# Kernel optimization log

Hardware: AMD Instinct MI355X
Metric: run time of the kernel (lower is better)

The kernel has to match this reference:

```python
import jax, jax.numpy as jnp
import numpy as np

DIM = 1024
D_STATE = 16
D_CONV = 4
EXPAND = 2
D_INNER = EXPAND * DIM          # 2048
DT_RANK = DIM // 16             # 64 (mamba default: ceil(d_model/16))
BATCH = 2
SEQ = 2048


def setup_inputs() -> dict:
    key = jax.random.key(0)
    ks = jax.random.split(key, 32)
    s = 0.02
    def mk(k, shape):
        return jax.random.normal(k, shape, jnp.float32) * s
    inp = {}
    inp["hidden_state"] = jax.random.normal(ks[0], (BATCH, SEQ, DIM), jnp.float32)
    inp["mask"] = jax.random.bernoulli(ks[1], 0.7, (BATCH, SEQ)).astype(jnp.float32)
    inp["mask_proj_w"] = mk(ks[2], (DIM, 1))
    inp["mask_proj_b"] = mk(ks[3], (DIM,))
    i = 4
    A_init = jnp.log(jnp.broadcast_to(jnp.arange(1, D_STATE + 1, dtype=jnp.float32), (D_INNER, D_STATE)))
    for p in ("f", "b"):
        inp[p + "_in_w"]   = mk(ks[i], (2 * D_INNER, DIM)); i += 1
        inp[p + "_conv_w"] = mk(ks[i], (D_INNER, D_CONV)); i += 1
        inp[p + "_conv_b"] = mk(ks[i], (D_INNER,)); i += 1
        inp[p + "_xproj_w"] = mk(ks[i], (DT_RANK + 2 * D_STATE, D_INNER)); i += 1
        inp[p + "_dt_w"]   = mk(ks[i], (D_INNER, DT_RANK)); i += 1
        inp[p + "_dt_b"]   = mk(ks[i], (D_INNER,)) + 1.0  # softplus(~1) -> moderate dt
        i += 1
        inp[p + "_A_log"]  = A_init
        inp[p + "_D"]      = jnp.ones((D_INNER,), jnp.float32)
        inp[p + "_out_w"]  = mk(ks[i], (DIM, D_INNER)); i += 1
    return inp


def _mamba(x, in_w, conv_w, conv_b, xproj_w, dt_w, dt_b, A_log, Dp, out_w):
    # x: [B, L, DIM]
    Bsz = x.shape[0]
    xz = x @ in_w.T                                  # [B, L, 2*D_INNER]
    xi, z = jnp.split(xz, 2, axis=-1)
    # causal depthwise conv1d over time
    xc = jnp.transpose(xi, (0, 2, 1))                # [B, D_INNER, L]
    xc = jax.lax.conv_general_dilated(
        xc, conv_w[:, None, :], window_strides=(1,),
        padding=[(D_CONV - 1, 0)], feature_group_count=D_INNER)
    xc = xc + conv_b[None, :, None]
    u = jax.nn.silu(jnp.transpose(xc, (0, 2, 1)))    # [B, L, D_INNER]
    dbc = u @ xproj_w.T                              # [B, L, DT_RANK + 2*D_STATE]
    dt, Bm, Cm = jnp.split(dbc, [DT_RANK, DT_RANK + D_STATE], axis=-1)
    delta = jax.nn.softplus(dt @ dt_w.T + dt_b)      # [B, L, D_INNER]
    A = -jnp.exp(A_log)                              # [D_INNER, D_STATE]
    dA = jnp.exp(jnp.einsum('bld,dn->bldn', delta, A))
    dBu = jnp.einsum('bld,bln,bld->bldn', delta, Bm, u)
    def step(h, inps):
        dA_t, dBu_t, C_t = inps                      # [B,D_INNER,D_STATE], [B,D_INNER,D_STATE], [B,D_STATE]
        h = dA_t * h + dBu_t
        y = jnp.einsum('bdn,bn->bd', h, C_t)
        return h, y
    h0 = jnp.zeros((Bsz, D_INNER, D_STATE), x.dtype)
    xs = (jnp.moveaxis(dA, 1, 0), jnp.moveaxis(dBu, 1, 0), jnp.moveaxis(Cm, 1, 0))
    _, ys = jax.lax.scan(step, h0, xs)               # ys: [L, B, D_INNER]
    y = jnp.moveaxis(ys, 0, 1) + u * Dp              # [B, L, D_INNER]
    y = y * jax.nn.silu(z)
    return y @ out_w.T                               # [B, L, DIM]


def reference(hidden_state, mask, mask_proj_w, mask_proj_b,
              f_in_w, f_conv_w, f_conv_b, f_xproj_w, f_dt_w, f_dt_b, f_A_log, f_D, f_out_w,
              b_in_w, b_conv_w, b_conv_b, b_xproj_w, b_dt_w, b_dt_b, b_A_log, b_D, b_out_w):
    m = mask[..., None]                              # [B, L, 1]
    mask_features = m @ mask_proj_w.T + mask_proj_b  # [B, L, DIM]
    x_masked = hidden_state * m + mask_features * (1.0 - m)
    forward_out = _mamba(x_masked, f_in_w, f_conv_w, f_conv_b, f_xproj_w,
                         f_dt_w, f_dt_b, f_A_log, f_D, f_out_w)
    backward_out = jnp.flip(
        _mamba(jnp.flip(x_masked, 1), b_in_w, b_conv_w, b_conv_b, b_xproj_w,
               b_dt_w, b_dt_b, b_A_log, b_D, b_out_w), 1)
    ssm_output = forward_out + backward_out
    return ssm_output * m + hidden_state * (1.0 - m)
```

## Files before the change

### kernel.cpp

```cpp
#include <hip/hip_runtime.h>
#include <hip/hip_bf16.h>
#include <stdint.h>

typedef unsigned short u16;
using bf16x8 = __attribute__((ext_vector_type(8))) short;
using f32x4  = __attribute__((ext_vector_type(4))) float;
typedef unsigned short u16x4 __attribute__((ext_vector_type(4)));

#define AS1 __attribute__((address_space(1)))
#define AS3 __attribute__((address_space(3)))

__device__ __forceinline__ float bf2f(u16 x) {
    union { unsigned int u; float f; } v; v.u = ((unsigned int)x) << 16; return v.f;
}
__device__ __forceinline__ u16 f2bf(float f) {
    union { float f; unsigned int u; } v; v.f = f;
    return (u16)((v.u + 0x7fffu + ((v.u >> 16) & 1u)) >> 16);
}

#define ACT_NONE 0
#define ACT_SOFTPLUS 1

__global__ __launch_bounds__(256) void gemm_bt_kernel(
    const u16* __restrict__ A, int lda,
    const u16* __restrict__ B,
    float* __restrict__ Cf, u16* __restrict__ Cb,
    const float* __restrict__ bias,
    int ldc, int M, int N, int K, int Nreal,
    int act, int kSlices,
    const float* __restrict__ hid, const float* __restrict__ msk)
{
    __shared__ __align__(16) u16 As[128 * 64];
    __shared__ __align__(16) u16 Bs[128 * 64];

    const int tid  = threadIdx.x;
    const int bm   = blockIdx.y * 128;
    const int bn   = blockIdx.x * 128;
    const int lane = tid & 63;
    const int wid  = tid >> 6;
    const int wr   = (wid >> 1) * 64;
    const int wc   = (wid & 1) * 64;
    const int l15  = lane & 15;
    const int l4   = lane >> 4;

    const int kLen = K / kSlices;
    const int kt0  = (blockIdx.z * kLen) >> 6;
    const int nK   = kLen >> 6;

    f32x4 acc[4][4];
    const f32x4 vzero = {0.f, 0.f, 0.f, 0.f};
    #pragma unroll
    for (int i = 0; i < 4; ++i)
        #pragma unroll
        for (int j = 0; j < 4; ++j) acc[i][j] = vzero;

    for (int t = 0; t < nK; ++t) {
        int kt = kt0 + t;
        #pragma unroll
        for (int i = 0; i < 4; ++i) {
            int off  = i * 4096 + tid * 16;
            int row  = off >> 7;
            int colB = off & 127;
            const char* src = (const char*)A + ((size_t)(bm + row) * lda + ((size_t)kt << 6)) * 2 + colB;
            __builtin_amdgcn_global_load_lds((const AS1 unsigned int*)src,
                                             (AS3 unsigned int*)((char*)As + off), 16, 0, 0);
        }
        #pragma unroll
        for (int i = 0; i < 4; ++i) {
            int off  = i * 4096 + tid * 16;
            int row  = off >> 7;
            int colB = off & 127;
            const char* src = (const char*)B + ((size_t)(bn + row) * K + ((size_t)kt << 6)) * 2 + colB;
            __builtin_amdgcn_global_load_lds((const AS1 unsigned int*)src,
                                             (AS3 unsigned int*)((char*)Bs + off), 16, 0, 0);
        }
        __syncthreads();

        #pragma unroll
        for (int kk = 0; kk < 2; ++kk) {
            bf16x8 af[4], bfr[4];
            #pragma unroll
            for (int mt = 0; mt < 4; ++mt) {
                int row = wr + mt * 16 + l15;
                af[mt] = *(const bf16x8*)((const char*)As + row * 128 + kk * 64 + l4 * 16);
            }
            #pragma unroll
            for (int nt = 0; nt < 4; ++nt) {
                int row = wc + nt * 16 + l15;
                bfr[nt] = *(const bf16x8*)((const char*)Bs + row * 128 + kk * 64 + l4 * 16);
            }
            #pragma unroll
            for (int mt = 0; mt < 4; ++mt)
                #pragma unroll
                for (int nt = 0; nt < 4; ++nt)
                    acc[mt][nt] = __builtin_amdgcn_mfma_f32_16x16x32_bf16(
                        af[mt], bfr[nt], acc[mt][nt], 0, 0, 0);
        }
        __syncthreads();
    }

    #pragma unroll
    for (int mt = 0; mt < 4; ++mt) {
        #pragma unroll
        for (int nt = 0; nt < 4; ++nt) {
            int col = bn + wc + nt * 16 + l15;
            if (col >= Nreal) continue;
            #pragma unroll
            for (int r = 0; r < 4; ++r) {
                int rw = bm + wr + mt * 16 + l4 * 4 + r;
                float v = acc[mt][nt][r];
                if (act == ACT_SOFTPLUS) {
                    v += bias[col];
                    v = fmaxf(v, 0.f) + log1pf(__expf(-fabsf(v)));
                }
                size_t ci = (size_t)rw * ldc + col;
                if (kSlices > 1) {
                    atomicAdd(&Cf[ci], v);
                } else if (hid) {
                    float m = msk[rw];
                    Cf[ci] = v * m + hid[ci] * (1.f - m);
                } else if (Cb) {
                    Cb[ci] = f2bf(v);
                } else {
                    Cf[ci] = v;
                }
            }
        }
    }
}

template<int REV>
__global__ void conv_silu_kernel(const u16* __restrict__ x,
                                 const float* __restrict__ cw,
                                 const float* __restrict__ cb,
                                 u16* __restrict__ u)
{
    int d  = blockIdx.x * 256 + threadIdx.x;
    int r0 = blockIdx.y * 16;
    float w0 = cw[d*4+0], w1 = cw[d*4+1], w2 = cw[d*4+2], w3 = cw[d*4+3];
    float bias = cb[d];
    if (!REV) {
        float x1, x2, x3;
        if (r0 & 2047) {
            x1 = bf2f(x[(size_t)(r0-1) * 8192 + d]);
            x2 = bf2f(x[(size_t)(r0-2) * 8192 + d]);
            x3 = bf2f(x[(size_t)(r0-3) * 8192 + d]);
        } else { x1 = x2 = x3 = 0.f; }
        #pragma unroll
        for (int i = 0; i < 16; ++i) {
            int r = r0 + i;
            float x0 = bf2f(x[(size_t)r * 8192 + d]);
            float acc = fmaf(w3, x0, fmaf(w2, x1, fmaf(w1, x2, fmaf(w0, x3, bias))));
            float sig = 1.f / (1.f + __expf(-acc));
            u[(size_t)r * 2048 + d] = f2bf(acc * sig);
            x3 = x2; x2 = x1; x1 = x0;
        }
    } else {
        int le = (r0 + 15) & 2047;
        float x1, x2, x3;
        x1 = (le + 1 < 2048) ? bf2f(x[(size_t)(r0+16) * 8192 + d]) : 0.f;
        x2 = (le + 2 < 2048) ? bf2f(x[(size_t)(r0+17) * 8192 + d]) : 0.f;
        x3 = (le + 3 < 2048) ? bf2f(x[(size_t)(r0+18) * 8192 + d]) : 0.f;
        #pragma unroll
        for (int i = 15; i >= 0; --i) {
            int r = r0 + i;
            float x0 = bf2f(x[(size_t)r * 8192 + d]);
            float acc = fmaf(w3, x0, fmaf(w2, x1, fmaf(w1, x2, fmaf(w0, x3, bias))));
            float sig = 1.f / (1.f + __expf(-acc));
            u[(size_t)r * 2048 + d] = f2bf(acc * sig);
            x3 = x2; x2 = x1; x1 = x0;
        }
    }
}

#define NCH 32
#define CSZ 64
#define SUB 16
#define LW  264

template<int REV>
__global__ __launch_bounds__(256) void scan_part1(
    const u16* __restrict__ delta, const u16* __restrict__ u,
    const float* __restrict__ dbc, const float* __restrict__ A_log,
    float* __restrict__ P, float* __restrict__ S)
{
    __shared__ __align__(16) u16   dl_s[SUB * LW];
    __shared__ __align__(16) u16   ul_s[SUB * LW];
    __shared__ __align__(16) float b_s[SUB * 16];

    const int tid = threadIdx.x;
    const int d0  = blockIdx.x * 256;
    const int c   = blockIdx.y;
    const int b   = blockIdx.z;
    const int d   = d0 + tid;
    const size_t rbase = (size_t)b * 2048 + c * CSZ;

    float a2[16], h[16], p[16];
    #pragma unroll
    for (int q = 0; q < 4; ++q) {
        float4 al = *(const float4*)&A_log[(size_t)d * 16 + q * 4];
        a2[q*4+0] = -__expf(al.x) * 1.4426950408889634f;
        a2[q*4+1] = -__expf(al.y) * 1.4426950408889634f;
        a2[q*4+2] = -__expf(al.z) * 1.4426950408889634f;
        a2[q*4+3] = -__expf(al.w) * 1.4426950408889634f;
    }
    #pragma unroll
    for (int n = 0; n < 16; ++n) { h[n] = 0.f; p[n] = 1.f; }

    const int sr  = tid >> 4;
    const int sc16 = (tid & 15) * 16;

    for (int sch = 0; sch < CSZ / SUB; ++sch) {
        const int sch_ = REV ? (CSZ / SUB - 1 - sch) : sch;
        {
            size_t row = rbase + sch_ * SUB + sr;
            *(bf16x8*)&dl_s[sr * LW + sc16]     = *(const bf16x8*)&delta[row * 2048 + d0 + sc16];
            *(bf16x8*)&dl_s[sr * LW + sc16 + 8] = *(const bf16x8*)&delta[row * 2048 + d0 + sc16 + 8];
            *(bf16x8*)&ul_s[sr * LW + sc16]     = *(const bf16x8*)&u[row * 2048 + d0 + sc16];
            *(bf16x8*)&ul_s[sr * LW + sc16 + 8] = *(const bf16x8*)&u[row * 2048 + d0 + sc16 + 8];
            if (tid < 64) {
                int r2 = tid >> 2, c4 = (tid & 3) * 4;
                size_t g2 = rbase + sch_ * SUB + r2;
                *(float4*)&b_s[r2 * 16 + c4] = *(const float4*)&dbc[g2 * 96 + 64 + c4];
            }
        }
        __syncthreads();
        for (int s = 0; s < SUB; ++s) {
            const int s_ = REV ? (SUB - 1 - s) : s;
            float dv  = bf2f(dl_s[s_ * LW + tid]);
            float uv  = bf2f(ul_s[s_ * LW + tid]);
            float dvu = dv * uv;
            const float4* Bp = (const float4*)&b_s[s_ * 16];
            #pragma unroll
            for (int q = 0; q < 4; ++q) {
                float4 Bq = Bp[q];
                #pragma unroll
                for (int j = 0; j < 4; ++j) {
                    int n = q * 4 + j;
                    float dA = exp2f(dv * a2[n]);
                    h[n] = fmaf(dA, h[n], dvu * ((&Bq.x)[j]));
                    p[n] *= dA;
                }
            }
        }
        __syncthreads();
    }

    size_t base = (((size_t)(b * NCH + c)) << 15) + (size_t)d * 16;
    #pragma unroll
    for (int q = 0; q < 4; ++q) {
        float4 pv = { p[q*4+0], p[q*4+1], p[q*4+2], p[q*4+3] };
        float4 sv = { h[q*4+0], h[q*4+1], h[q*4+2], h[q*4+3] };
        *(float4*)&P[base + q * 4] = pv;
        *(float4*)&S[base + q * 4] = sv;
    }
}

template<int REV>
__global__ void scan_part2(const float* __restrict__ P, float* __restrict__ S)
{
    int i  = blockIdx.x * 256 + threadIdx.x;
    int b  = i >> 15;
    int dn = i & 32767;
    size_t base = ((size_t)b * NCH) << 15;
    float h = 0.f;
    #pragma unroll 4
    for (int cc = 0; cc < NCH; ++cc) {
        int c = REV ? (NCH - 1 - cc) : cc;
        size_t idx = base + ((size_t)c << 15) + dn;
        float p = P[idx];
        float s = S[idx];
        S[idx] = h;
        h = fmaf(p, h, s);
    }
}

template<int REV>
__global__ __launch_bounds__(256) void scan_part3(
    const u16* __restrict__ delta, const u16* __restrict__ u,
    const float* __restrict__ dbc, const u16* __restrict__ z,
    const float* __restrict__ A_log, const float* __restrict__ Dp,
    const float* __restrict__ Hin, u16* __restrict__ y)
{
    __shared__ __align__(16) u16   dl_s[SUB * LW];
    __shared__ __align__(16) u16   ul_s[SUB * LW];
    __shared__ __align__(16) u16   zl_s[SUB * LW];
    __shared__ __align__(16) float bc_s[SUB * 32];

    const int tid = threadIdx.x;
    const int d0  = blockIdx.x * 256;
    const int c   = blockIdx.y;
    const int b   = blockIdx.z;
    const int d   = d0 + tid;
    const size_t rbase = (size_t)b * 2048 + c * CSZ;

    float a2[16], h[16];
    #pragma unroll
    for (int q = 0; q < 4; ++q) {
        float4 al = *(const float4*)&A_log[(size_t)d * 16 + q * 4];
        a2[q*4+0] = -__expf(al.x) * 1.4426950408889634f;
        a2[q*4+1] = -__expf(al.y) * 1.4426950408889634f;
        a2[q*4+2] = -__expf(al.z) * 1.4426950408889634f;
        a2[q*4+3] = -__expf(al.w) * 1.4426950408889634f;
    }
    {
        size_t base = (((size_t)(b * NCH + c)) << 15) + (size_t)d * 16;
        #pragma unroll
        for (int q = 0; q < 4; ++q) {
            float4 hv = *(const float4*)&Hin[base + q * 4];
            h[q*4+0] = hv.x; h[q*4+1] = hv.y; h[q*4+2] = hv.z; h[q*4+3] = hv.w;
        }
    }
    const float Dd = Dp[d];

    const int sr   = tid >> 4;
    const int sc16 = (tid & 15) * 16;

    for (int sch = 0; sch < CSZ / SUB; ++sch) {
        const int sch_ = REV ? (CSZ / SUB - 1 - sch) : sch;
        {
            size_t row = rbase + sch_ * SUB + sr;
            *(bf16x8*)&dl_s[sr * LW + sc16]     = *(const bf16x8*)&delta[row * 2048 + d0 + sc16];
            *(bf16x8*)&dl_s[sr * LW + sc16 + 8] = *(const bf16x8*)&delta[row * 2048 + d0 + sc16 + 8];
            *(bf16x8*)&ul_s[sr * LW + sc16]     = *(const bf16x8*)&u[row * 2048 + d0 + sc16];
            *(bf16x8*)&ul_s[sr * LW + sc16 + 8] = *(const bf16x8*)&u[row * 2048 + d0 + sc16 + 8];
            *(bf16x8*)&zl_s[sr * LW + sc16]     = *(const bf16x8*)&z[row * 8192 + d0 + sc16];
            *(bf16x8*)&zl_s[sr * LW + sc16 + 8] = *(const bf16x8*)&z[row * 8192 + d0 + sc16 + 8];
            if (tid < 128) {
                int r2 = tid >> 3, c4 = (tid & 7) * 4;
                size_t g2 = rbase + sch_ * SUB + r2;
                *(float4*)&bc_s[r2 * 32 + c4] = *(const float4*)&dbc[g2 * 96 + 64 + c4];
            }
        }
        __syncthreads();
        for (int s = 0; s < SUB; ++s) {
            const int s_ = REV ? (SUB - 1 - s) : s;
            float dv  = bf2f(dl_s[s_ * LW + tid]);
            float uv  = bf2f(ul_s[s_ * LW + tid]);
            float dvu = dv * uv;
            float yv  = 0.f;
            const float4* Bp = (const float4*)&bc_s[s_ * 32];
            const float4* Cp = (const float4*)&bc_s[s_ * 32 + 16];
            #pragma unroll
            for (int q = 0; q < 4; ++q) {
                float4 Bq = Bp[q];
                float4 Cq = Cp[q];
                #pragma unroll
                for (int j = 0; j < 4; ++j) {
                    int n = q * 4 + j;
                    float dA = exp2f(dv * a2[n]);
                    h[n] = fmaf(dA, h[n], dvu * ((&Bq.x)[j]));
                    yv   = fmaf(h[n], ((&Cq.x)[j]), yv);
                }
            }
            float zv  = bf2f(zl_s[s_ * LW + tid]);
            float sig = 1.f / (1.f + __expf(-zv));
            float out = (yv + uv * Dd) * (zv * sig);
            y[(rbase + sch_ * SUB + s_) * 4096 + d] = f2bf(out);
        }
        __syncthreads();
    }
}

__global__ void blend_kernel(const float* __restrict__ hidden, const float* __restrict__ mask,
                             const float* __restrict__ mw, const float* __restrict__ mb,
                             u16* __restrict__ xm)
{
    size_t i = (size_t)blockIdx.x * 256 + threadIdx.x;
    int r = (int)(i >> 10), c = (int)(i & 1023);
    float m = mask[r];
    float v = hidden[i] * m + (m * mw[c] + mb[c]) * (1.f - m);
    xm[i] = f2bf(v);
}

struct CvtArgs { const float* src[8]; u16* dst[8]; };
__global__ void cvt_weights_kernel(CvtArgs a)
{
    size_t i = (size_t)blockIdx.x * 256 + threadIdx.x;
    if (i < 8388608) {
        int s = (int)(i >> 22);
        size_t j = i & 4194303;
        a.dst[0][i] = f2bf(a.src[s][j]);
    } else if (i < 12582912) {
        size_t k = i - 8388608;
        int s = (int)(k >> 21);
        size_t j = k & 2097151;
        int n = (int)(j >> 11), kk = (int)(j & 2047);
        a.dst[2][(size_t)n * 4096 + s * 2048 + kk] = f2bf(a.src[2 + s][j]);
    } else if (i < 12845056) {
        size_t k = i - 12582912;
        int s = 4 + (int)(k >> 17);
        size_t j = k & 131071;
        a.dst[s][j] = f2bf(a.src[s][j]);
    } else if (i < 13369344) {
        size_t k = i - 12845056;
        int s = 6 + (int)(k >> 18);
        size_t j = k & 262143;
        int r = (int)(j >> 11), c = (int)(j & 2047);
        a.dst[s][j] = (r < 96) ? f2bf(a.src[s][(size_t)r * 2048 + c]) : (u16)0;
    }
}

__global__ void cvt_dt_kernel(const float* __restrict__ dbc, u16* __restrict__ dst) {
    int i = blockIdx.x * 256 + threadIdx.x;
    int r = i >> 6, c = i & 63;
    dst[i] = f2bf(dbc[(size_t)r * 96 + c]);
}

extern "C" void kernel_launch(void* const* d_in, const int* in_sizes, int n_in,
                              void* d_out, int out_size, void* d_ws, size_t ws_size,
                              hipStream_t stream)
{
    (void)in_sizes; (void)n_in; (void)out_size; (void)ws_size;
    const float* hidden = (const float*)d_in[0];
    const float* mask   = (const float*)d_in[1];
    const float* mpw    = (const float*)d_in[2];
    const float* mpb    = (const float*)d_in[3];

    char* ws = (char*)d_ws;
    size_t off = 0;
    auto alloc = [&](size_t bytes) -> char* {
        char* p = ws + off; off += (bytes + 255) & ~(size_t)255; return p;
    };
    u16*   xm     = (u16*)  alloc(4096ull * 1024 * 2);
    u16*   xz     = (u16*)  alloc(4096ull * 8192 * 2);
    u16*   ub     = (u16*)  alloc(4096ull * 2048 * 2);
    float* dbc    = (float*)alloc(4096ull * 96 * 4);
    u16*   dtb    = (u16*)  alloc(4096ull * 64 * 2);
    u16*   delta  = (u16*)  alloc(4096ull * 2048 * 2);
    u16*   yb     = (u16*)  alloc(4096ull * 4096 * 2);
    float* Pbuf   = (float*)alloc(2ull * NCH * 2048 * 16 * 4);
    float* Sbuf   = (float*)alloc(2ull * NCH * 2048 * 16 * 4);
    u16*   w_in   = (u16*)  alloc(8192ull * 1024 * 2);
    u16*   w_out  = (u16*)  alloc(1024ull * 4096 * 2);
    u16*   w_xp[2] = { (u16*)alloc(128ull*2048*2), (u16*)alloc(128ull*2048*2) };
    u16*   w_dt[2] = { (u16*)alloc(2048ull*64*2),  (u16*)alloc(2048ull*64*2)  };

    {
        CvtArgs ca;
        ca.src[0] = (const float*)d_in[4];  ca.src[1] = (const float*)d_in[13];
        ca.src[2] = (const float*)d_in[12]; ca.src[3] = (const float*)d_in[21];
        ca.src[4] = (const float*)d_in[8];  ca.src[5] = (const float*)d_in[17];
        ca.src[6] = (const float*)d_in[7];  ca.src[7] = (const float*)d_in[16];
        ca.dst[0] = w_in;  ca.dst[1] = nullptr;
        ca.dst[2] = w_out; ca.dst[3] = nullptr;
        ca.dst[4] = w_dt[0]; ca.dst[5] = w_dt[1];
        ca.dst[6] = w_xp[0]; ca.dst[7] = w_xp[1];
        cvt_weights_kernel<<<(13369344 + 255) / 256, 256, 0, stream>>>(ca);
    }
    blend_kernel<<<16384, 256, 0, stream>>>(hidden, mask, mpw, mpb, xm);

    gemm_bt_kernel<<<dim3(64, 32, 1), 256, 0, stream>>>(
        xm, 1024, w_in, nullptr, xz, nullptr, 8192, 4096, 8192, 1024, 8192,
        ACT_NONE, 1, nullptr, nullptr);

    for (int dir = 0; dir < 2; ++dir) {
        int base = 4 + dir * 9;
        const float* conv_w = (const float*)d_in[base+1];
        const float* conv_b = (const float*)d_in[base+2];
        const float* dt_b   = (const float*)d_in[base+5];
        const float* A_log  = (const float*)d_in[base+6];
        const float* Dp     = (const float*)d_in[base+7];
        const u16* xi = xz + dir * 4096;
        const u16* zp = xz + dir * 4096 + 2048;

        if (dir == 0) conv_silu_kernel<0><<<dim3(8, 256), 256, 0, stream>>>(xi, conv_w, conv_b, ub);
        else          conv_silu_kernel<1><<<dim3(8, 256), 256, 0, stream>>>(xi, conv_w, conv_b, ub);

        hipMemsetAsync(dbc, 0, 4096ull * 96 * 4, stream);
        gemm_bt_kernel<<<dim3(1, 32, 4), 256, 0, stream>>>(
            ub, 2048, w_xp[dir], dbc, nullptr, nullptr, 96, 4096, 128, 2048, 96,
            ACT_NONE, 4, nullptr, nullptr);
        cvt_dt_kernel<<<(4096*64)/256, 256, 0, stream>>>(dbc, dtb);
        gemm_bt_kernel<<<dim3(16, 32, 1), 256, 0, stream>>>(
            dtb, 64, w_dt[dir], nullptr, delta, dt_b, 2048, 4096, 2048, 64, 2048,
            ACT_SOFTPLUS, 1, nullptr, nullptr);

        u16* yd = yb + dir * 2048;
        if (dir == 0) {
            scan_part1<0><<<dim3(8, NCH, 2), 256, 0, stream>>>(delta, ub, dbc, A_log, Pbuf, Sbuf);
            scan_part2<0><<<256, 256, 0, stream>>>(Pbuf, Sbuf);
            scan_part3<0><<<dim3(8, NCH, 2), 256, 0, stream>>>(delta, ub, dbc, zp, A_log, Dp, Sbuf, yd);
        } else {
            scan_part1<1><<<dim3(8, NCH, 2), 256, 0, stream>>>(delta, ub, dbc, A_log, Pbuf, Sbuf);
            scan_part2<1><<<256, 256, 0, stream>>>(Pbuf, Sbuf);
            scan_part3<1><<<dim3(8, NCH, 2), 256, 0, stream>>>(delta, ub, dbc, zp, A_log, Dp, Sbuf, yd);
        }
    }

    gemm_bt_kernel<<<dim3(8, 32, 1), 256, 0, stream>>>(
        yb, 4096, w_out, (float*)d_out, nullptr, nullptr, 1024, 4096, 1024, 4096, 1024,
        ACT_NONE, 1, hidden, mask);
}
```

Baseline: 763.1 us.

## Batch forward and backward directions into single dual-direction kernel launches

Merges the per-direction conv, x-proj GEMM, dt GEMM and three scan kernels into launches that cover both directions through the grid z dimension. It also folds the blend into the weight-conversion kernel and writes delta into the unused xi slot of xz. The aim is to cut launch count and raise occupancy for the small under-filled kernels such as the scan, x-proj and part2. The cost is duplicated buffers for u, dbc and P/S, plus per-block pointer selection logic.

```diff
diff --git a/kernel.cpp b/kernel.cpp
--- a/kernel.cpp
+++ b/kernel.cpp
@@ -5,7 +5,6 @@
 typedef unsigned short u16;
 using bf16x8 = __attribute__((ext_vector_type(8))) short;
 using f32x4  = __attribute__((ext_vector_type(4))) float;
-typedef unsigned short u16x4 __attribute__((ext_vector_type(4)));
 
 #define AS1 __attribute__((address_space(1)))
 #define AS3 __attribute__((address_space(3)))
@@ -20,6 +19,11 @@
 
 #define ACT_NONE 0
 #define ACT_SOFTPLUS 1
+
+struct GemmSel {
+    const u16* A1; const u16* B1;
+    float* Cf1; u16* Cb1; const float* bias1;
+};
 
 __global__ __launch_bounds__(256) void gemm_bt_kernel(
     const u16* __restrict__ A, int lda,
@@ -27,8 +31,9 @@
     float* __restrict__ Cf, u16* __restrict__ Cb,
     const float* __restrict__ bias,
     int ldc, int M, int N, int K, int Nreal,
-    int act, int kSlices,
-    const float* __restrict__ hid, const float* __restrict__ msk)
+    int act, int kSlices, int zDiv,
+    const float* __restrict__ hid, const float* __restrict__ msk,
+    GemmSel sel)
 {
     __shared__ __align__(16) u16 As[128 * 64];
     __shared__ __align__(16) u16 Bs[128 * 64];
@@ -43,8 +48,16 @@
     const int l15  = lane & 15;
     const int l4   = lane >> 4;
 
+    const int dir   = blockIdx.z / zDiv;
+    const int slice = blockIdx.z % zDiv;
+    const u16* Ap = (dir && sel.A1) ? sel.A1 : A;
+    const u16* Bp = (dir && sel.B1) ? sel.B1 : B;
+    float* CfP = (dir && sel.Cf1) ? sel.Cf1 : Cf;
+    u16*   CbP = (dir && sel.Cb1) ? sel.Cb1 : Cb;
+    const float* biasP = (dir && sel.bias1) ? sel.bias1 : bias;
+
     const int kLen = K / kSlices;
-    const int kt0  = (blockIdx.z * kLen) >> 6;
+    const int kt0  = (slice * kLen) >> 6;
     const int nK   = kLen >> 6;
 
     f32x4 acc[4][4];
@@ -61,7 +74,7 @@
             int off  = i * 4096 + tid * 16;
             int row  = off >> 7;
             int colB = off & 127;
-            const char* src = (const char*)A + ((size_t)(bm + row) * lda + ((size_t)kt << 6)) * 2 + colB;
+            const char* src = (const char*)Ap + ((size_t)(bm + row) * lda + ((size_t)kt << 6)) * 2 + colB;
             __builtin_amdgcn_global_load_lds((const AS1 unsigned int*)src,
                                              (AS3 unsigned int*)((char*)As + off), 16, 0, 0);
         }
@@ -70,7 +83,7 @@
             int off  = i * 4096 + tid * 16;
             int row  = off >> 7;
             int colB = off & 127;
-            const char* src = (const char*)B + ((size_t)(bn + row) * K + ((size_t)kt << 6)) * 2 + colB;
+            const char* src = (const char*)Bp + ((size_t)(bn + row) * K + ((size_t)kt << 6)) * 2 + colB;
             __builtin_amdgcn_global_load_lds((const AS1 unsigned int*)src,
                                              (AS3 unsigned int*)((char*)Bs + off), 16, 0, 0);
         }
@@ -110,36 +123,39 @@
                 int rw = bm + wr + mt * 16 + l4 * 4 + r;
                 float v = acc[mt][nt][r];
                 if (act == ACT_SOFTPLUS) {
-                    v += bias[col];
+                    v += biasP[col];
                     v = fmaxf(v, 0.f) + log1pf(__expf(-fabsf(v)));
                 }
                 size_t ci = (size_t)rw * ldc + col;
                 if (kSlices > 1) {
-                    atomicAdd(&Cf[ci], v);
+                    atomicAdd(&CfP[ci], v);
                 } else if (hid) {
                     float m = msk[rw];
-                    Cf[ci] = v * m + hid[ci] * (1.f - m);
-                } else if (Cb) {
-                    Cb[ci] = f2bf(v);
+                    CfP[ci] = v * m + hid[ci] * (1.f - m);
+                } else if (CbP) {
+                    CbP[ci] = f2bf(v);
                 } else {
-                    Cf[ci] = v;
+                    CfP[ci] = v;
                 }
             }
         }
     }
 }
 
-template<int REV>
-__global__ void conv_silu_kernel(const u16* __restrict__ x,
-                                 const float* __restrict__ cw,
-                                 const float* __restrict__ cb,
-                                 u16* __restrict__ u)
-{
+struct ConvArgs { const float* cw[2]; const float* cb[2]; u16* u[2]; };
+__global__ void conv_silu_dual(const u16* __restrict__ xz, ConvArgs a)
+{
+    const int dir = blockIdx.z;
+    const u16* x = xz + dir * 4096;
+    const float* cw = a.cw[dir];
+    const float* cb = a.cb[dir];
+    u16* u = a.u[dir];
+
     int d  = blockIdx.x * 256 + threadIdx.x;
     int r0 = blockIdx.y * 16;
     float w0 = cw[d*4+0], w1 = cw[d*4+1], w2 = cw[d*4+2], w3 = cw[d*4+3];
     float bias = cb[d];
-    if (!REV) {
+    if (dir == 0) {
         float x1, x2, x3;
         if (r0 & 2047) {
             x1 = bf2f(x[(size_t)(r0-1) * 8192 + d]);
@@ -178,11 +194,18 @@
 #define SUB 16
 #define LW  264
 
-template<int REV>
-__global__ __launch_bounds__(256) void scan_part1(
-    const u16* __restrict__ delta, const u16* __restrict__ u,
-    const float* __restrict__ dbc, const float* __restrict__ A_log,
-    float* __restrict__ P, float* __restrict__ S)
+struct ScanArgs {
+    const u16* delta[2];
+    const u16* u[2];
+    const float* dbc[2];
+    const u16* z[2];
+    const float* Alog[2];
+    const float* Dp[2];
+    float* P[2]; float* S[2];
+    u16* y[2];
+};
+
+__global__ __launch_bounds__(256) void scan_part1_dual(ScanArgs sa)
 {
     __shared__ __align__(16) u16   dl_s[SUB * LW];
     __shared__ __align__(16) u16   ul_s[SUB * LW];
@@ -191,14 +214,20 @@
     const int tid = threadIdx.x;
     const int d0  = blockIdx.x * 256;
     const int c   = blockIdx.y;
-    const int b   = blockIdx.z;
+    const int dir = blockIdx.z >> 1;
+    const int b   = blockIdx.z & 1;
+    const int rev = dir;
     const int d   = d0 + tid;
     const size_t rbase = (size_t)b * 2048 + c * CSZ;
+
+    const u16* D = sa.delta[dir];
+    const u16* U = sa.u[dir];
+    const float* BC = sa.dbc[dir];
 
     float a2[16], h[16], p[16];
     #pragma unroll
     for (int q = 0; q < 4; ++q) {
-        float4 al = *(const float4*)&A_log[(size_t)d * 16 + q * 4];
+        float4 al = *(const float4*)&sa.Alog[dir][(size_t)d * 16 + q * 4];
         a2[q*4+0] = -__expf(al.x) * 1.4426950408889634f;
         a2[q*4+1] = -__expf(al.y) * 1.4426950408889634f;
         a2[q*4+2] = -__expf(al.z) * 1.4426950408889634f;
@@ -211,22 +240,22 @@
     const int sc16 = (tid & 15) * 16;
 
     for (int sch = 0; sch < CSZ / SUB; ++sch) {
-        const int sch_ = REV ? (CSZ / SUB - 1 - sch) : sch;
+        const int sch_ = rev ? (CSZ / SUB - 1 - sch) : sch;
         {
             size_t row = rbase + sch_ * SUB + sr;
-            *(bf16x8*)&dl_s[sr * LW + sc16]     = *(const bf16x8*)&delta[row * 2048 + d0 + sc16];
-            *(bf16x8*)&dl_s[sr * LW + sc16 + 8] = *(const bf16x8*)&delta[row * 2048 + d0 + sc16 + 8];
-            *(bf16x8*)&ul_s[sr * LW + sc16]     = *(const bf16x8*)&u[row * 2048 + d0 + sc16];
-            *(bf16x8*)&ul_s[sr * LW + sc16 + 8] = *(const bf16x8*)&u[row * 2048 + d0 + sc16 + 8];
+            *(bf16x8*)&dl_s[sr * LW + sc16]     = *(const bf16x8*)&D[row * 8192 + d0 + sc16];
+            *(bf16x8*)&dl_s[sr * LW + sc16 + 8] = *(const bf16x8*)&D[row * 8192 + d0 + sc16 + 8];
+            *(bf16x8*)&ul_s[sr * LW + sc16]     = *(const bf16x8*)&U[row * 2048 + d0 + sc16];
+            *(bf16x8*)&ul_s[sr * LW + sc16 + 8] = *(const bf16x8*)&U[row * 2048 + d0 + sc16 + 8];
             if (tid < 64) {
                 int r2 = tid >> 2, c4 = (tid & 3) * 4;
                 size_t g2 = rbase + sch_ * SUB + r2;
-                *(float4*)&b_s[r2 * 16 + c4] = *(const float4*)&dbc[g2 * 96 + 64 + c4];
+                *(float4*)&b_s[r2 * 16 + c4] = *(const float4*)&BC[g2 * 96 + 64 + c4];
             }
         }
         __syncthreads();
         for (int s = 0; s < SUB; ++s) {
-            const int s_ = REV ? (SUB - 1 - s) : s;
+            const int s_ = rev ? (SUB - 1 - s) : s;
             float dv  = bf2f(dl_s[s_ * LW + tid]);
             float uv  = bf2f(ul_s[s_ * LW + tid]);
             float dvu = dv * uv;
@@ -251,22 +280,25 @@
     for (int q = 0; q < 4; ++q) {
         float4 pv = { p[q*4+0], p[q*4+1], p[q*4+2], p[q*4+3] };
         float4 sv = { h[q*4+0], h[q*4+1], h[q*4+2], h[q*4+3] };
-        *(float4*)&P[base + q * 4] = pv;
-        *(float4*)&S[base + q * 4] = sv;
-    }
-}
-
-template<int REV>
-__global__ void scan_part2(const float* __restrict__ P, float* __restrict__ S)
-{
-    int i  = blockIdx.x * 256 + threadIdx.x;
-    int b  = i >> 15;
-    int dn = i & 32767;
+        *(float4*)&sa.P[dir][base + q * 4] = pv;
+        *(float4*)&sa.S[dir][base + q * 4] = sv;
+    }
+}
+
+__global__ void scan_part2_dual(ScanArgs sa)
+{
+    int i   = blockIdx.x * 256 + threadIdx.x;
+    int dir = i >> 16;
+    int k   = i & 65535;
+    int b   = k >> 15;
+    int dn  = k & 32767;
+    const float* P = sa.P[dir];
+    float* S = sa.S[dir];
     size_t base = ((size_t)b * NCH) << 15;
     float h = 0.f;
     #pragma unroll 4
     for (int cc = 0; cc < NCH; ++cc) {
-        int c = REV ? (NCH - 1 - cc) : cc;
+        int c = dir ? (NCH - 1 - cc) : cc;
         size_t idx = base + ((size_t)c << 15) + dn;
         float p = P[idx];
         float s = S[idx];
@@ -275,12 +307,7 @@
     }
 }
 
-template<int REV>
-__global__ __launch_bounds__(256) void scan_part3(
-    const u16* __restrict__ delta, const u16* __restrict__ u,
-    const float* __restrict__ dbc, const u16* __restrict__ z,
-    const float* __restrict__ A_log, const float* __restrict__ Dp,
-    const float* __restrict__ Hin, u16* __restrict__ y)
+__global__ __launch_bounds__(256) void scan_part3_dual(ScanArgs sa)
 {
     __shared__ __align__(16) u16   dl_s[SUB * LW];
     __shared__ __align__(16) u16   ul_s[SUB * LW];
@@ -290,14 +317,22 @@
     const int tid = threadIdx.x;
     const int d0  = blockIdx.x * 256;
     const int c   = blockIdx.y;
-    const int b   = blockIdx.z;
+    const int dir = blockIdx.z >> 1;
+    const int b   = blockIdx.z & 1;
+    const int rev = dir;
     const int d   = d0 + tid;
     const size_t rbase = (size_t)b * 2048 + c * CSZ;
+
+    const u16* D = sa.delta[dir];
+    const u16* U = sa.u[dir];
+    const float* BC = sa.dbc[dir];
+    const u16* Z = sa.z[dir];
+    u16* Y = sa.y[dir];
 
     float a2[16], h[16];
     #pragma unroll
     for (int q = 0; q < 4; ++q) {
-        float4 al = *(const float4*)&A_log[(size_t)d * 16 + q * 4];
+        float4 al = *(const float4*)&sa.Alog[dir][(size_t)d * 16 + q * 4];
         a2[q*4+0] = -__expf(al.x) * 1.4426950408889634f;
         a2[q*4+1] = -__expf(al.y) * 1.4426950408889634f;
         a2[q*4+2] = -__expf(al.z) * 1.4426950408889634f;
@@ -307,34 +342,34 @@
         size_t base = (((size_t)(b * NCH + c)) << 15) + (size_t)d * 16;
         #pragma unroll
         for (int q = 0; q < 4; ++q) {
-            float4 hv = *(const float4*)&Hin[base + q * 4];
+            float4 hv = *(const float4*)&sa.S[dir][base + q * 4];
             h[q*4+0] = hv.x; h[q*4+1] = hv.y; h[q*4+2] = hv.z; h[q*4+3] = hv.w;
         }
     }
-    const float Dd = Dp[d];
+    const float Dd = sa.Dp[dir][d];
 
     const int sr   = tid >> 4;
     const int sc16 = (tid & 15) * 16;
 
     for (int sch = 0; sch < CSZ / SUB; ++sch) {
-        const int sch_ = REV ? (CSZ / SUB - 1 - sch) : sch;
+        const int sch_ = rev ? (CSZ / SUB - 1 - sch) : sch;
         {
             size_t row = rbase + sch_ * SUB + sr;
-            *(bf16x8*)&dl_s[sr * LW + sc16]     = *(const bf16x8*)&delta[row * 2048 + d0 + sc16];
-            *(bf16x8*)&dl_s[sr * LW + sc16 + 8] = *(const bf16x8*)&delta[row * 2048 + d0 + sc16 + 8];
-            *(bf16x8*)&ul_s[sr * LW + sc16]     = *(const bf16x8*)&u[row * 2048 + d0 + sc16];
-            *(bf16x8*)&ul_s[sr * LW + sc16 + 8] = *(const bf16x8*)&u[row * 2048 + d0 + sc16 + 8];
-            *(bf16x8*)&zl_s[sr * LW + sc16]     = *(const bf16x8*)&z[row * 8192 + d0 + sc16];
-            *(bf16x8*)&zl_s[sr * LW + sc16 + 8] = *(const bf16x8*)&z[row * 8192 + d0 + sc16 + 8];
+            *(bf16x8*)&dl_s[sr * LW + sc16]     = *(const bf16x8*)&D[row * 8192 + d0 + sc16];
+            *(bf16x8*)&dl_s[sr * LW + sc16 + 8] = *(const bf16x8*)&D[row * 8192 + d0 + sc16 + 8];
+            *(bf16x8*)&ul_s[sr * LW + sc16]     = *(const bf16x8*)&U[row * 2048 + d0 + sc16];
+            *(bf16x8*)&ul_s[sr * LW + sc16 + 8] = *(const bf16x8*)&U[row * 2048 + d0 + sc16 + 8];
+            *(bf16x8*)&zl_s[sr * LW + sc16]     = *(const bf16x8*)&Z[row * 8192 + d0 + sc16];
+            *(bf16x8*)&zl_s[sr * LW + sc16 + 8] = *(const bf16x8*)&Z[row * 8192 + d0 + sc16 + 8];
             if (tid < 128) {
                 int r2 = tid >> 3, c4 = (tid & 7) * 4;
                 size_t g2 = rbase + sch_ * SUB + r2;
-                *(float4*)&bc_s[r2 * 32 + c4] = *(const float4*)&dbc[g2 * 96 + 64 + c4];
+                *(float4*)&bc_s[r2 * 32 + c4] = *(const float4*)&BC[g2 * 96 + 64 + c4];
             }
         }
         __syncthreads();
         for (int s = 0; s < SUB; ++s) {
-            const int s_ = REV ? (SUB - 1 - s) : s;
+            const int s_ = rev ? (SUB - 1 - s) : s;
             float dv  = bf2f(dl_s[s_ * LW + tid]);
             float uv  = bf2f(ul_s[s_ * LW + tid]);
             float dvu = dv * uv;
@@ -356,55 +391,59 @@
             float zv  = bf2f(zl_s[s_ * LW + tid]);
             float sig = 1.f / (1.f + __expf(-zv));
             float out = (yv + uv * Dd) * (zv * sig);
-            y[(rbase + sch_ * SUB + s_) * 4096 + d] = f2bf(out);
+            Y[(rbase + sch_ * SUB + s_) * 4096 + d] = f2bf(out);
         }
         __syncthreads();
     }
 }
 
-__global__ void blend_kernel(const float* __restrict__ hidden, const float* __restrict__ mask,
-                             const float* __restrict__ mw, const float* __restrict__ mb,
-                             u16* __restrict__ xm)
-{
-    size_t i = (size_t)blockIdx.x * 256 + threadIdx.x;
-    int r = (int)(i >> 10), c = (int)(i & 1023);
-    float m = mask[r];
-    float v = hidden[i] * m + (m * mw[c] + mb[c]) * (1.f - m);
-    xm[i] = f2bf(v);
-}
-
-struct CvtArgs { const float* src[8]; u16* dst[8]; };
-__global__ void cvt_weights_kernel(CvtArgs a)
+struct PrepArgs {
+    const float* src_in[2]; const float* src_out[2];
+    const float* src_dt[2]; const float* src_xp[2];
+    u16* w_in; u16* w_out; u16* w_dt[2]; u16* w_xp[2];
+    const float* hidden; const float* mask; const float* mw; const float* mb;
+    u16* xm;
+};
+__global__ void prep_kernel(PrepArgs a)
 {
     size_t i = (size_t)blockIdx.x * 256 + threadIdx.x;
     if (i < 8388608) {
         int s = (int)(i >> 22);
         size_t j = i & 4194303;
-        a.dst[0][i] = f2bf(a.src[s][j]);
+        a.w_in[i] = f2bf(a.src_in[s][j]);
     } else if (i < 12582912) {
         size_t k = i - 8388608;
         int s = (int)(k >> 21);
         size_t j = k & 2097151;
         int n = (int)(j >> 11), kk = (int)(j & 2047);
-        a.dst[2][(size_t)n * 4096 + s * 2048 + kk] = f2bf(a.src[2 + s][j]);
+        a.w_out[(size_t)n * 4096 + s * 2048 + kk] = f2bf(a.src_out[s][j]);
     } else if (i < 12845056) {
         size_t k = i - 12582912;
-        int s = 4 + (int)(k >> 17);
+        int s = (int)(k >> 17);
         size_t j = k & 131071;
-        a.dst[s][j] = f2bf(a.src[s][j]);
+        a.w_dt[s][j] = f2bf(a.src_dt[s][j]);
     } else if (i < 13369344) {
         size_t k = i - 12845056;
-        int s = 6 + (int)(k >> 18);
+        int s = (int)(k >> 18);
         size_t j = k & 262143;
         int r = (int)(j >> 11), c = (int)(j & 2047);
-        a.dst[s][j] = (r < 96) ? f2bf(a.src[s][(size_t)r * 2048 + c]) : (u16)0;
-    }
-}
-
-__global__ void cvt_dt_kernel(const float* __restrict__ dbc, u16* __restrict__ dst) {
+        a.w_xp[s][j] = (r < 96) ? f2bf(a.src_xp[s][(size_t)r * 2048 + c]) : (u16)0;
+    } else if (i < 17563648) {
+        size_t k = i - 13369344;
+        int r = (int)(k >> 10), c = (int)(k & 1023);
+        float m = a.mask[r];
+        float v = a.hidden[k] * m + (m * a.mw[c] + a.mb[c]) * (1.f - m);
+        a.xm[k] = f2bf(v);
+    }
+}
+
+__global__ void cvt_dt_dual(const float* __restrict__ dbc, u16* __restrict__ dtb)
+{
     int i = blockIdx.x * 256 + threadIdx.x;
-    int r = i >> 6, c = i & 63;
-    dst[i] = f2bf(dbc[(size_t)r * 96 + c]);
+    int dir = i >> 18;
+    int j = i & 262143;
+    int r = j >> 6, c = j & 63;
+    dtb[i] = f2bf(dbc[(size_t)dir * 4096 * 96 + (size_t)r * 96 + c]);
 }
 
 extern "C" void kernel_launch(void* const* d_in, const int* in_sizes, int n_in,
@@ -414,81 +453,93 @@
     (void)in_sizes; (void)n_in; (void)out_size; (void)ws_size;
     const float* hidden = (const float*)d_in[0];
     const float* mask   = (const float*)d_in[1];
-    const float* mpw    = (const float*)d_in[2];
-    const float* mpb    = (const float*)d_in[3];
 
     char* ws = (char*)d_ws;
     size_t off = 0;
     auto alloc = [&](size_t bytes) -> char* {
         char* p = ws + off; off += (bytes + 255) & ~(size_t)255; return p;
     };
-    u16*   xm     = (u16*)  alloc(4096ull * 1024 * 2);
-    u16*   xz     = (u16*)  alloc(4096ull * 8192 * 2);
-    u16*   ub     = (u16*)  alloc(4096ull * 2048 * 2);
-    float* dbc    = (float*)alloc(4096ull * 96 * 4);
-    u16*   dtb    = (u16*)  alloc(4096ull * 64 * 2);
-    u16*   delta  = (u16*)  alloc(4096ull * 2048 * 2);
-    u16*   yb     = (u16*)  alloc(4096ull * 4096 * 2);
-    float* Pbuf   = (float*)alloc(2ull * NCH * 2048 * 16 * 4);
-    float* Sbuf   = (float*)alloc(2ull * NCH * 2048 * 16 * 4);
-    u16*   w_in   = (u16*)  alloc(8192ull * 1024 * 2);
-    u16*   w_out  = (u16*)  alloc(1024ull * 4096 * 2);
-    u16*   w_xp[2] = { (u16*)alloc(128ull*2048*2), (u16*)alloc(128ull*2048*2) };
-    u16*   w_dt[2] = { (u16*)alloc(2048ull*64*2),  (u16*)alloc(2048ull*64*2)  };
+    u16*   xm    = (u16*)  alloc(4096ull * 1024 * 2);
+    u16*   xz    = (u16*)  alloc(4096ull * 8192 * 2);
+    u16*   ub0   = (u16*)  alloc(4096ull * 2048 * 2);
+    u16*   ub1   = (u16*)  alloc(4096ull * 2048 * 2);
+    float* dbc   = (float*)alloc(2ull * 4096 * 96 * 4);
+    u16*   dtb   = (u16*)  alloc(2ull * 4096 * 64 * 2);
+    u16*   yb    = (u16*)  alloc(4096ull * 4096 * 2);
+    float* Pbuf  = (float*)alloc(2ull * 2 * NCH * 2048 * 16 * 4);
+    float* Sbuf  = (float*)alloc(2ull * 2 * NCH * 2048 * 16 * 4);
+    u16*   w_in  = (u16*)  alloc(8192ull * 1024 * 2);
+    u16*   w_out = (u16*)  alloc(1024ull * 4096 * 2);
+    u16*   w_xp0 = (u16*)  alloc(128ull * 2048 * 2);
+    u16*   w_xp1 = (u16*)  alloc(128ull * 2048 * 2);
+    u16*   w_dt0 = (u16*)  alloc(2048ull * 64 * 2);
+    u16*   w_dt1 = (u16*)  alloc(2048ull * 64 * 2);
+
+    const size_t PS_DIR = 2ull * NCH * 2048 * 16;
 
     {
-        CvtArgs ca;
-        ca.src[0] = (const float*)d_in[4];  ca.src[1] = (const float*)d_in[13];
-        ca.src[2] = (const float*)d_in[12]; ca.src[3] = (const float*)d_in[21];
-        ca.src[4] = (const float*)d_in[8];  ca.src[5] = (const float*)d_in[17];
-        ca.src[6] = (const float*)d_in[7];  ca.src[7] = (const float*)d_in[16];
-        ca.dst[0] = w_in;  ca.dst[1] = nullptr;
-        ca.dst[2] = w_out; ca.dst[3] = nullptr;
-        ca.dst[4] = w_dt[0]; ca.dst[5] = w_dt[1];
-        ca.dst[6] = w_xp[0]; ca.dst[7] = w_xp[1];
-        cvt_weights_kernel<<<(13369344 + 255) / 256, 256, 0, stream>>>(ca);
-    }
-    blend_kernel<<<16384, 256, 0, stream>>>(hidden, mask, mpw, mpb, xm);
+        PrepArgs pa;
+        pa.src_in[0]  = (const float*)d_in[4];  pa.src_in[1]  = (const float*)d_in[13];
+        pa.src_out[0] = (const float*)d_in[12]; pa.src_out[1] = (const float*)d_in[21];
+        pa.src_dt[0]  = (const float*)d_in[8];  pa.src_dt[1]  = (const float*)d_in[17];
+        pa.src_xp[0]  = (const float*)d_in[7];  pa.src_xp[1]  = (const float*)d_in[16];
+        pa.w_in = w_in; pa.w_out = w_out;
+        pa.w_dt[0] = w_dt0; pa.w_dt[1] = w_dt1;
+        pa.w_xp[0] = w_xp0; pa.w_xp[1] = w_xp1;
+        pa.hidden = hidden; pa.mask = mask;
+        pa.mw = (const float*)d_in[2]; pa.mb = (const float*)d_in[3];
+        pa.xm = xm;
+        prep_kernel<<<(17563648 + 255) / 256, 256, 0, stream>>>(pa);
+    }
+
+    GemmSel nosel = {nullptr, nullptr, nullptr, nullptr, nullptr};
 
     gemm_bt_kernel<<<dim3(64, 32, 1), 256, 0, stream>>>(
         xm, 1024, w_in, nullptr, xz, nullptr, 8192, 4096, 8192, 1024, 8192,
-        ACT_NONE, 1, nullptr, nullptr);
-
-    for (int dir = 0; dir < 2; ++dir) {
-        int base = 4 + dir * 9;
-        const float* conv_w = (const float*)d_in[base+1];
-        const float* conv_b = (const float*)d_in[base+2];
-        const float* dt_b   = (const float*)d_in[base+5];
-        const float* A_log  = (const float*)d_in[base+6];
-        const float* Dp     = (const float*)d_in[base+7];
-        const u16* xi = xz + dir * 4096;
-        const u16* zp = xz + dir * 4096 + 2048;
-
-        if (dir == 0) conv_silu_kernel<0><<<dim3(8, 256), 256, 0, stream>>>(xi, conv_w, conv_b, ub);
-        else          conv_silu_kernel<1><<<dim3(8, 256), 256, 0, stream>>>(xi, conv_w, conv_b, ub);
-
-        hipMemsetAsync(dbc, 0, 4096ull * 96 * 4, stream);
-        gemm_bt_kernel<<<dim3(1, 32, 4), 256, 0, stream>>>(
-            ub, 2048, w_xp[dir], dbc, nullptr, nullptr, 96, 4096, 128, 2048, 96,
-            ACT_NONE, 4, nullptr, nullptr);
-        cvt_dt_kernel<<<(4096*64)/256, 256, 0, stream>>>(dbc, dtb);
-        gemm_bt_kernel<<<dim3(16, 32, 1), 256, 0, stream>>>(
-            dtb, 64, w_dt[dir], nullptr, delta, dt_b, 2048, 4096, 2048, 64, 2048,
-            ACT_SOFTPLUS, 1, nullptr, nullptr);
-
-        u16* yd = yb + dir * 2048;
-        if (dir == 0) {
-            scan_part1<0><<<dim3(8, NCH, 2), 256, 0, stream>>>(delta, ub, dbc, A_log, Pbuf, Sbuf);
-            scan_part2<0><<<256, 256, 0, stream>>>(Pbuf, Sbuf);
-            scan_part3<0><<<dim3(8, NCH, 2), 256, 0, stream>>>(delta, ub, dbc, zp, A_log, Dp, Sbuf, yd);
-        } else {
-            scan_part1<1><<<dim3(8, NCH, 2), 256, 0, stream>>>(delta, ub, dbc, A_log, Pbuf, Sbuf);
-            scan_part2<1><<<256, 256, 0, stream>>>(Pbuf, Sbuf);
-            scan_part3<1><<<dim3(8, NCH, 2), 256, 0, stream>>>(delta, ub, dbc, zp, A_log, Dp, Sbuf, yd);
-        }
+        ACT_NONE, 1, 1, nullptr, nullptr, nosel);
+
+    {
+        ConvArgs ca;
+        ca.cw[0] = (const float*)d_in[5];  ca.cw[1] = (const float*)d_in[14];
+        ca.cb[0] = (const float*)d_in[6];  ca.cb[1] = (const float*)d_in[15];
+        ca.u[0] = ub0; ca.u[1] = ub1;
+        conv_silu_dual<<<dim3(8, 256, 2), 256, 0, stream>>>(xz, ca);
+    }
+
+    hipMemsetAsync(dbc, 0, 2ull * 4096 * 96 * 4, stream);
+    {
+        GemmSel sel = {ub1, w_xp1, dbc + 4096 * 96, nullptr, nullptr};
+        gemm_bt_kernel<<<dim3(1, 32, 8), 256, 0, stream>>>(
+            ub0, 2048, w_xp0, dbc, nullptr, nullptr, 96, 4096, 128, 2048, 96,
+            ACT_NONE, 4, 4, nullptr, nullptr, sel);
+    }
+
+    cvt_dt_dual<<<524288 / 256, 256, 0, stream>>>(dbc, dtb);
+
+    {
+        GemmSel sel = {dtb + 262144, w_dt1, nullptr, xz + 4096, (const float*)d_in[18]};
+        gemm_bt_kernel<<<dim3(16, 32, 2), 256, 0, stream>>>(
+            dtb, 64, w_dt0, nullptr, xz, (const float*)d_in[9], 8192, 4096, 2048, 64, 2048,
+            ACT_SOFTPLUS, 1, 1, nullptr, nullptr, sel);
+    }
+
+    {
+        ScanArgs sa;
+        sa.delta[0] = xz;            sa.delta[1] = xz + 4096;
+        sa.u[0] = ub0;               sa.u[1] = ub1;
+        sa.dbc[0] = dbc;             sa.dbc[1] = dbc + 4096 * 96;
+        sa.z[0] = xz + 2048;         sa.z[1] = xz + 4096 + 2048;
+        sa.Alog[0] = (const float*)d_in[10]; sa.Alog[1] = (const float*)d_in[19];
+        sa.Dp[0]   = (const float*)d_in[11]; sa.Dp[1]   = (const float*)d_in[20];
+        sa.P[0] = Pbuf;              sa.P[1] = Pbuf + PS_DIR;
+        sa.S[0] = Sbuf;              sa.S[1] = Sbuf + PS_DIR;
+        sa.y[0] = yb;                sa.y[1] = yb + 2048;
+        scan_part1_dual<<<dim3(8, NCH, 4), 256, 0, stream>>>(sa);
+        scan_part2_dual<<<512, 256, 0, stream>>>(sa);
+        scan_part3_dual<<<dim3(8, NCH, 4), 256, 0, stream>>>(sa);
     }
 
     gemm_bt_kernel<<<dim3(8, 32, 1), 256, 0, stream>>>(
         yb, 4096, w_out, (float*)d_out, nullptr, nullptr, 1024, 4096, 1024, 4096, 1024,
-        ACT_NONE, 1, hidden, mask);
-}
+        ACT_NONE, 1, 1, hidden, mask, nosel);
+}
```

Result: faster. 703.9 us (-7.8%).
